# Kernel tuning notes

Hardware: AMD Instinct MI355X
Metric: run time of the kernel (lower is better)

## Reference

```python
import jax, jax.numpy as jnp
import numpy as np

NC, NP_, E = 100000, 50000, 500000
DC, DP = 256, 128
HID, OUT = 64, 64
H1, H2 = 2, 1
SLOPE = 0.2


def setup_inputs() -> dict:
    key = jax.random.key(0)
    ks = jax.random.split(key, 32)
    d = {}
    d['x_customer'] = jax.random.normal(ks[0], (NC, DC), jnp.float32)
    d['x_product'] = jax.random.normal(ks[1], (NP_, DP), jnp.float32)
    d['edge_src'] = jax.random.randint(ks[2], (E,), 0, NC, jnp.int32)
    d['edge_dst'] = jax.random.randint(ks[3], (E,), 0, NP_, jnp.int32)
    s = 0.1
    # layer1, edge type (customer, buys, product): src=customer, dst=product
    d['w1b_src'] = jax.random.normal(ks[4], (DC, H1 * HID)) * s
    d['w1b_dst'] = jax.random.normal(ks[5], (DP, H1 * HID)) * s
    d['a1b_src'] = jax.random.normal(ks[6], (H1, HID)) * s
    d['a1b_dst'] = jax.random.normal(ks[7], (H1, HID)) * s
    d['b1b'] = jnp.zeros((H1 * HID,), jnp.float32)
    # layer1, edge type (product, rev_buys, customer): src=product, dst=customer
    d['w1r_src'] = jax.random.normal(ks[8], (DP, H1 * HID)) * s
    d['w1r_dst'] = jax.random.normal(ks[9], (DC, H1 * HID)) * s
    d['a1r_src'] = jax.random.normal(ks[10], (H1, HID)) * s
    d['a1r_dst'] = jax.random.normal(ks[11], (H1, HID)) * s
    d['b1r'] = jnp.zeros((H1 * HID,), jnp.float32)
    # layer2 (input dim = H1*HID = 128 for both node types), heads=1
    d['w2b_src'] = jax.random.normal(ks[12], (H1 * HID, H2 * OUT)) * s
    d['w2b_dst'] = jax.random.normal(ks[13], (H1 * HID, H2 * OUT)) * s
    d['a2b_src'] = jax.random.normal(ks[14], (H2, OUT)) * s
    d['a2b_dst'] = jax.random.normal(ks[15], (H2, OUT)) * s
    d['b2b'] = jnp.zeros((H2 * OUT,), jnp.float32)
    d['w2r_src'] = jax.random.normal(ks[16], (H1 * HID, H2 * OUT)) * s
    d['w2r_dst'] = jax.random.normal(ks[17], (H1 * HID, H2 * OUT)) * s
    d['a2r_src'] = jax.random.normal(ks[18], (H2, OUT)) * s
    d['a2r_dst'] = jax.random.normal(ks[19], (H2, OUT)) * s
    d['b2r'] = jnp.zeros((H2 * OUT,), jnp.float32)
    return d


def _gat_conv(h_src, h_dst, e_src, e_dst, att_src, att_dst, bias, n_dst):
    # h_src: [Ns,H,C] projected source feats; h_dst: [Nd,H,C]
    a_s = (h_src * att_src).sum(-1)  # [Ns,H]
    a_d = (h_dst * att_dst).sum(-1)  # [Nd,H]
    alpha = jax.nn.leaky_relu(a_s[e_src] + a_d[e_dst], negative_slope=SLOPE)  # [E,H]
    m = jax.lax.stop_gradient(jax.ops.segment_max(alpha, e_dst, num_segments=n_dst))
    ex = jnp.exp(alpha - m[e_dst])
    den = jax.ops.segment_sum(ex, e_dst, num_segments=n_dst)
    w = ex / (den[e_dst] + 1e-16)  # segment softmax over incoming edges
    msg = h_src[e_src] * w[..., None]  # [E,H,C]
    out = jax.ops.segment_sum(msg, e_dst, num_segments=n_dst)  # [Nd,H,C]
    return out.reshape(n_dst, -1) + bias


def reference(x_customer, x_product, edge_src, edge_dst,
              w1b_src, w1b_dst, a1b_src, a1b_dst, b1b,
              w1r_src, w1r_dst, a1r_src, a1r_dst, b1r,
              w2b_src, w2b_dst, a2b_src, a2b_dst, b2b,
              w2r_src, w2r_dst, a2r_src, a2r_dst, b2r):
    # ---- layer 1 (heads=2, concat) ----
    hs = (x_customer @ w1b_src).reshape(NC, H1, HID)
    hd = (x_product @ w1b_dst).reshape(NP_, H1, HID)
    p1 = _gat_conv(hs, hd, edge_src, edge_dst, a1b_src, a1b_dst, b1b, NP_)
    hs = (x_product @ w1r_src).reshape(NP_, H1, HID)
    hd = (x_customer @ w1r_dst).reshape(NC, H1, HID)
    c1 = _gat_conv(hs, hd, edge_dst, edge_src, a1r_src, a1r_dst, b1r, NC)
    c1 = jax.nn.relu(c1)
    p1 = jax.nn.relu(p1)
    # ---- layer 2 (heads=1) ----
    hs = (c1 @ w2b_src).reshape(NC, H2, OUT)
    hd = (p1 @ w2b_dst).reshape(NP_, H2, OUT)
    p2 = _gat_conv(hs, hd, edge_src, edge_dst, a2b_src, a2b_dst, b2b, NP_)
    hs = (p1 @ w2r_src).reshape(NP_, H2, OUT)
    hd = (c1 @ w2r_dst).reshape(NC, H2, OUT)
    c2 = _gat_conv(hs, hd, edge_dst, edge_src, a2r_src, a2r_dst, b2r, NC)
    return c2, p2
```

## Files before the change

kernel.cpp:

```cpp
#include <hip/hip_runtime.h>
#include <hip/hip_bf16.h>

typedef __bf16 bf16_t;
typedef bf16_t bf16x2 __attribute__((ext_vector_type(2)));
typedef bf16_t bf16x4 __attribute__((ext_vector_type(4)));
typedef bf16_t bf16x8 __attribute__((ext_vector_type(8)));
typedef float f32x2 __attribute__((ext_vector_type(2)));
typedef float f32x4 __attribute__((ext_vector_type(4)));

static constexpr int NCn = 100000;
static constexpr int NPn = 50000;
static constexpr int NE  = 500000;

__device__ __forceinline__ float ldin(const void* p, size_t i, int fp32) {
    return fp32 ? ((const float*)p)[i] : (float)((const bf16_t*)p)[i];
}

__global__ __launch_bounds__(256) void prep_meta(const void* x, int* flag,
                                                 const void* w1bd, const void* a1bd,
                                                 const void* w1rd, const void* a1rd,
                                                 const void* w2bd, const void* a2bd,
                                                 const void* w2rd, const void* a2rd,
                                                 float* V1bd, float* V1rd,
                                                 float* V2bd, float* V2rd) {
    __shared__ int sflag;
    int t = threadIdx.x;
    if (t < 64) {
        const bf16_t* xb = (const bf16_t*)x;
        int bad = 0;
        for (int i = t; i < 512; i += 64) {
            float v = (float)xb[i];
            if (!(v > -1e4f && v < 1e4f)) bad = 1;
        }
        unsigned long long m = __ballot(bad);
        if (t == 0) { sflag = (m != 0ull) ? 1 : 0; flag[0] = sflag; }
    }
    __syncthreads();
    int fp32 = sflag;
    for (int idx = t; idx < 256; idx += 256) {
        int k = idx >> 1, h = idx & 1;
        float s = 0.f;
        for (int c = 0; c < 64; ++c)
            s += ldin(w1bd, (size_t)k * 128 + h * 64 + c, fp32) * ldin(a1bd, h * 64 + c, fp32);
        V1bd[k * 2 + h] = s;
    }
    for (int idx = t; idx < 512; idx += 256) {
        int k = idx >> 1, h = idx & 1;
        float s = 0.f;
        for (int c = 0; c < 64; ++c)
            s += ldin(w1rd, (size_t)k * 128 + h * 64 + c, fp32) * ldin(a1rd, h * 64 + c, fp32);
        V1rd[k * 2 + h] = s;
    }
    for (int k = t; k < 128; k += 256) {
        float s = 0.f;
        for (int c = 0; c < 64; ++c)
            s += ldin(w2bd, (size_t)k * 64 + c, fp32) * ldin(a2bd, c, fp32);
        V2bd[k] = s;
    }
    for (int k = t; k < 128; k += 256) {
        float s = 0.f;
        for (int c = 0; c < 64; ++c)
            s += ldin(w2rd, (size_t)k * 64 + c, fp32) * ldin(a2rd, c, fp32);
        V2rd[k] = s;
    }
}

__global__ __launch_bounds__(256) void prep_w4(const void* __restrict__ w1b, bf16_t* __restrict__ Wt1b,
                                               const void* __restrict__ w1r, bf16_t* __restrict__ Wt1r,
                                               const void* __restrict__ w2b, bf16_t* __restrict__ Wt2b,
                                               const void* __restrict__ w2r, bf16_t* __restrict__ Wt2r,
                                               const int* __restrict__ flag) {
    int fp32 = flag[0];
    int b = blockIdx.x;
    const void* W; bf16_t* Wt; int N, ks, base;
    if (b < 128)      { W = w1b; Wt = Wt1b; N = 128; ks = 8; base = 0;   }
    else if (b < 192) { W = w1r; Wt = Wt1r; N = 128; ks = 7; base = 128; }
    else if (b < 224) { W = w2b; Wt = Wt2b; N = 64;  ks = 7; base = 192; }
    else              { W = w2r; Wt = Wt2r; N = 64;  ks = 7; base = 224; }
    int idx = (b - base) * 256 + threadIdx.x;
    int K = 1 << ks;
    int n = idx >> ks, k = idx & (K - 1);
    if (n < N) Wt[idx] = (bf16_t)ldin(W, (size_t)k * N + n, fp32);
}

template<int K>
__device__ __forceinline__ void cvt_body(const void* __restrict__ X,
                                         bf16_t* __restrict__ Xb,
                                         const float* __restrict__ V,
                                         float* __restrict__ ad,
                                         int M, int fp32, int blk) {
    constexpr int EPL = K / 64;
    int wid = (blk * 256 + (int)threadIdx.x) >> 6;
    int lane = threadIdx.x & 63;
    if (wid >= M) return;
    size_t base = (size_t)wid * K + lane * EPL;
    float x[EPL];
    if constexpr (EPL == 4) {
        if (fp32) { f32x4 t = *(const f32x4*)((const float*)X + base);
#pragma unroll
            for (int j = 0; j < 4; ++j) x[j] = t[j];
        } else { bf16x4 t = *(const bf16x4*)((const bf16_t*)X + base);
#pragma unroll
            for (int j = 0; j < 4; ++j) x[j] = (float)t[j];
        }
        bf16x4 o;
#pragma unroll
        for (int j = 0; j < 4; ++j) o[j] = (bf16_t)x[j];
        *(bf16x4*)(Xb + base) = o;
    } else {
        if (fp32) { f32x2 t = *(const f32x2*)((const float*)X + base);
#pragma unroll
            for (int j = 0; j < 2; ++j) x[j] = t[j];
        } else { bf16x2 t = *(const bf16x2*)((const bf16_t*)X + base);
#pragma unroll
            for (int j = 0; j < 2; ++j) x[j] = (float)t[j];
        }
        bf16x2 o;
#pragma unroll
        for (int j = 0; j < 2; ++j) o[j] = (bf16_t)x[j];
        *(bf16x2*)(Xb + base) = o;
    }
    float a0 = 0.f, a1 = 0.f;
#pragma unroll
    for (int j = 0; j < EPL; ++j) {
        int k = lane * EPL + j;
        a0 += x[j] * V[k * 2];
        a1 += x[j] * V[k * 2 + 1];
    }
    for (int off = 32; off; off >>= 1) {
        a0 += __shfl_down(a0, off);
        a1 += __shfl_down(a1, off);
    }
    if (lane == 0) { ad[(size_t)wid * 2] = a0; ad[(size_t)wid * 2 + 1] = a1; }
}

__global__ __launch_bounds__(256) void cvt2(const void* __restrict__ Xc, bf16_t* __restrict__ Xcb,
                                            const float* __restrict__ Vc, float* __restrict__ adc,
                                            const void* __restrict__ Xp, bf16_t* __restrict__ Xpb,
                                            const float* __restrict__ Vp, float* __restrict__ adp,
                                            int gC, const int* __restrict__ flag) {
    int fp32 = flag[0];
    if ((int)blockIdx.x < gC) cvt_body<256>(Xc, Xcb, Vc, adc, NCn, fp32, blockIdx.x);
    else                      cvt_body<128>(Xp, Xpb, Vp, adp, NPn, fp32, blockIdx.x - gC);
}

__global__ __launch_bounds__(256) void zero2(int* __restrict__ a, int na,
                                             int* __restrict__ b, int nb) {
    int i = blockIdx.x * 256 + threadIdx.x;
    if (i < na) a[i] = 0;
    else if (i - na < nb) b[i - na] = 0;
}

__global__ __launch_bounds__(256) void hist2(const int* __restrict__ esrc,
                                             const int* __restrict__ edst,
                                             int* __restrict__ cntR,
                                             int* __restrict__ cntB, int E) {
    int e = blockIdx.x * 256 + threadIdx.x;
    if (e >= E) return;
    atomicAdd(&cntB[edst[e]], 1);
    atomicAdd(&cntR[esrc[e]], 1);
}

__global__ __launch_bounds__(256) void scan_blocks2(const int* __restrict__ cntB, int* __restrict__ rsB,
                                                    int* __restrict__ bsumB, int NB, int sbB,
                                                    const int* __restrict__ cntR, int* __restrict__ rsR,
                                                    int* __restrict__ bsumR, int NR) {
    const int* cnt; int* rs; int* bsum; int N; int b;
    if ((int)blockIdx.x < sbB) { cnt = cntB; rs = rsB; bsum = bsumB; N = NB; b = blockIdx.x; }
    else { cnt = cntR; rs = rsR; bsum = bsumR; N = NR; b = blockIdx.x - sbB; }
    int t = threadIdx.x;
    int base = b * 1024 + t * 4;
    int c[4];
#pragma unroll
    for (int k = 0; k < 4; ++k) { int i = base + k; c[k] = (i < N) ? cnt[i] : 0; }
    int tsum = c[0] + c[1] + c[2] + c[3];
    __shared__ int sd[256];
    sd[t] = tsum;
    __syncthreads();
    for (int off = 1; off < 256; off <<= 1) {
        int x = (t >= off) ? sd[t - off] : 0;
        __syncthreads();
        sd[t] += x;
        __syncthreads();
    }
    int run = sd[t] - tsum;
#pragma unroll
    for (int k = 0; k < 4; ++k) { int i = base + k; if (i < N) rs[i] = run; run += c[k]; }
    if (t == 255) bsum[b] = sd[255];
}

__global__ __launch_bounds__(128) void scan_bsum2(int* __restrict__ bsumB, int nbB,
                                                  int* __restrict__ bsumR, int nbR) {
    int* bsum = blockIdx.x ? bsumR : bsumB;
    int nb = blockIdx.x ? nbR : nbB;
    int t = threadIdx.x;
    __shared__ int sd[128];
    int v = (t < nb) ? bsum[t] : 0;
    sd[t] = v;
    __syncthreads();
    for (int off = 1; off < 128; off <<= 1) {
        int x = (t >= off) ? sd[t - off] : 0;
        __syncthreads();
        sd[t] += x;
        __syncthreads();
    }
    if (t < nb) bsum[t] = sd[t] - v;
}

__global__ __launch_bounds__(256) void scan_add2(int* __restrict__ rsB, const int* __restrict__ bsumB,
                                                 int NB, int* __restrict__ cntB,
                                                 int* __restrict__ rsR, const int* __restrict__ bsumR,
                                                 int NR, int* __restrict__ cntR, int E) {
    int i = blockIdx.x * 256 + threadIdx.x;
    if (i < NB) { int v = rsB[i] + bsumB[i >> 10]; rsB[i] = v; cntB[i] = v; }
    if (i < NR) { int v = rsR[i] + bsumR[i >> 10]; rsR[i] = v; cntR[i] = v; }
    if (i == 0) { rsB[NB] = E; rsR[NR] = E; }
}

__global__ __launch_bounds__(256) void scatter2(const int* __restrict__ esrc,
                                                const int* __restrict__ edst,
                                                int* __restrict__ curB, int* __restrict__ curR,
                                                int* __restrict__ srcsB, int* __restrict__ dstsB,
                                                int* __restrict__ srcsR, int* __restrict__ dstsR,
                                                int E) {
    int e = blockIdx.x * 256 + threadIdx.x;
    if (e >= E) return;
    int s = esrc[e], d = edst[e];
    int pb = atomicAdd(&curB[d], 1);
    srcsB[pb] = s; dstsB[pb] = d;
    int pr = atomicAdd(&curR[s], 1);
    srcsR[pr] = d; dstsR[pr] = s;
}

template<int K, int NT, int H>
__device__ __forceinline__ void gemm_body(const bf16_t* __restrict__ A,
                                          const bf16_t* __restrict__ Wt,
                                          bf16_t* __restrict__ C,
                                          const void* __restrict__ att,
                                          float* __restrict__ asout,
                                          int M, int fp32, int bx) {
    constexpr int N = NT * 16;
    const int w = threadIdx.x >> 6;
    const int lane = threadIdx.x & 63;
    const int lm = lane & 15;
    const int lq = lane >> 4;
    const int r0 = bx * 128 + w * 32;
    int ra0 = r0 + lm;       if (ra0 > M - 1) ra0 = M - 1;
    int ra1 = r0 + 16 + lm;  if (ra1 > M - 1) ra1 = M - 1;
    const bf16_t* A0 = A + (size_t)ra0 * K + lq * 8;
    const bf16_t* A1 = A + (size_t)ra1 * K + lq * 8;
    const bf16_t* B0 = Wt + (size_t)lm * K + lq * 8;
    f32x4 acc[2][NT] = {};
#pragma unroll
    for (int kt = 0; kt < K / 32; ++kt) {
        bf16x8 a0 = *(const bf16x8*)(A0 + kt * 32);
        bf16x8 a1 = *(const bf16x8*)(A1 + kt * 32);
#pragma unroll
        for (int nt = 0; nt < NT; ++nt) {
            bf16x8 b = *(const bf16x8*)(B0 + (size_t)nt * 16 * K + kt * 32);
            acc[0][nt] = __builtin_amdgcn_mfma_f32_16x16x32_bf16(a0, b, acc[0][nt], 0, 0, 0);
            acc[1][nt] = __builtin_amdgcn_mfma_f32_16x16x32_bf16(a1, b, acc[1][nt], 0, 0, 0);
        }
    }
#pragma unroll
    for (int rt = 0; rt < 2; ++rt) {
        const int crow0 = r0 + rt * 16 + lq * 4;
#pragma unroll
        for (int nt = 0; nt < NT; ++nt) {
            int col = nt * 16 + lm;
#pragma unroll
            for (int i = 0; i < 4; ++i) {
                int r = crow0 + i;
                if (r < M) C[(size_t)r * N + col] = (bf16_t)acc[rt][nt][i];
            }
        }
    }
    float attv[NT];
#pragma unroll
    for (int nt = 0; nt < NT; ++nt) attv[nt] = ldin(att, nt * 16 + lm, fp32);
    float p0[2][4], p1[2][4];
#pragma unroll
    for (int rt = 0; rt < 2; ++rt)
#pragma unroll
        for (int i = 0; i < 4; ++i) {
            float s0 = 0.f, s1 = 0.f;
#pragma unroll
            for (int nt = 0; nt < NT; ++nt) {
                if (H == 2 && nt >= 4) s1 += acc[rt][nt][i] * attv[nt];
                else                   s0 += acc[rt][nt][i] * attv[nt];
            }
            p0[rt][i] = s0; p1[rt][i] = s1;
        }
#pragma unroll
    for (int off = 1; off < 16; off <<= 1)
#pragma unroll
        for (int rt = 0; rt < 2; ++rt)
#pragma unroll
            for (int i = 0; i < 4; ++i) {
                p0[rt][i] += __shfl_xor(p0[rt][i], off);
                if (H == 2) p1[rt][i] += __shfl_xor(p1[rt][i], off);
            }
    if (lm == 0) {
#pragma unroll
        for (int rt = 0; rt < 2; ++rt)
#pragma unroll
            for (int i = 0; i < 4; ++i) {
                int r = r0 + rt * 16 + lq * 4 + i;
                if (r < M) {
                    asout[(size_t)r * H] = p0[rt][i];
                    if (H == 2) asout[(size_t)r * H + 1] = p1[rt][i];
                }
            }
    }
}

__global__ __launch_bounds__(256) void gemm_l1(const bf16_t* __restrict__ xcb, const bf16_t* __restrict__ Wt1b,
                                               bf16_t* __restrict__ Hc, const void* __restrict__ a1b, float* __restrict__ as_b,
                                               const bf16_t* __restrict__ xpb, const bf16_t* __restrict__ Wt1r,
                                               bf16_t* __restrict__ Hp, const void* __restrict__ a1r, float* __restrict__ as_r,
                                               int gmC, const int* __restrict__ flag) {
    int fp32 = flag[0];
    if ((int)blockIdx.x < gmC)
        gemm_body<256, 8, 2>(xcb, Wt1b, Hc, a1b, as_b, NCn, fp32, blockIdx.x);
    else
        gemm_body<128, 8, 2>(xpb, Wt1r, Hp, a1r, as_r, NPn, fp32, blockIdx.x - gmC);
}

__global__ __launch_bounds__(256) void gemm_l2(const bf16_t* __restrict__ c1, const bf16_t* __restrict__ Wt2b,
                                               bf16_t* __restrict__ Hc2, const void* __restrict__ a2b, float* __restrict__ as2c,
                                               const bf16_t* __restrict__ p1, const bf16_t* __restrict__ Wt2r,
                                               bf16_t* __restrict__ Hp2, const void* __restrict__ a2r, float* __restrict__ as2p,
                                               int gmC, const int* __restrict__ flag) {
    int fp32 = flag[0];
    if ((int)blockIdx.x < gmC)
        gemm_body<128, 4, 1>(c1, Wt2b, Hc2, a2b, as2c, NCn, fp32, blockIdx.x);
    else
        gemm_body<128, 4, 1>(p1, Wt2r, Hp2, a2r, as2p, NPn, fp32, blockIdx.x - gmC);
}

template<int H>
__global__ __launch_bounds__(256) void edge_pk2(const int* __restrict__ srcsB,
                                                const int* __restrict__ dstsB,
                                                const float* __restrict__ asB,
                                                const float* __restrict__ adB,
                                                float* __restrict__ pkB,
                                                const int* __restrict__ srcsR,
                                                const int* __restrict__ dstsR,
                                                const float* __restrict__ asR,
                                                const float* __restrict__ adR,
                                                float* __restrict__ pkR,
                                                int gE, int E) {
    const int *srcs, *dsts; const float *as_, *ad_; float* pk; int j;
    if ((int)blockIdx.x < gE) {
        j = blockIdx.x * 256 + threadIdx.x;
        srcs = srcsB; dsts = dstsB; as_ = asB; ad_ = adB; pk = pkB;
    } else {
        j = (blockIdx.x - gE) * 256 + threadIdx.x;
        srcs = srcsR; dsts = dstsR; as_ = asR; ad_ = adR; pk = pkR;
    }
    if (j >= E) return;
    int s = srcs[j], d = dsts[j];
    if constexpr (H == 2) {
        f32x2 a = *(const f32x2*)(as_ + 2 * (size_t)s);
        f32x2 b = *(const f32x2*)(ad_ + 2 * (size_t)d);
        float v0 = a[0] + b[0]; v0 = v0 > 0.f ? v0 : 0.2f * v0;
        float v1 = a[1] + b[1]; v1 = v1 > 0.f ? v1 : 0.2f * v1;
        f32x4 o;
        o[0] = __uint_as_float((unsigned)s << 8);
        o[1] = __expf(fminf(v0, 60.f));
        o[2] = __expf(fminf(v1, 60.f));
        o[3] = 0.f;
        *(f32x4*)(pk + 4 * (size_t)j) = o;
    } else {
        float v = as_[s] + ad_[d];
        v = v > 0.f ? v : 0.2f * v;
        f32x2 o;
        o[0] = __uint_as_float((unsigned)s << 7);
        o[1] = __expf(fminf(v, 60.f));
        *(f32x2*)(pk + 2 * (size_t)j) = o;
    }
}

template<int HD, int MODE>
__global__ __launch_bounds__(256) void aggregate2(
        const int* __restrict__ rsB, const float* __restrict__ pkB,
        const bf16_t* __restrict__ HmB, const void* __restrict__ biasB,
        const float* __restrict__ V2B, float* __restrict__ ad2B,
        void* __restrict__ outB, size_t obaseB, int NdB,
        const int* __restrict__ rsR, const float* __restrict__ pkR,
        const bf16_t* __restrict__ HmR, const void* __restrict__ biasR,
        const float* __restrict__ V2R, float* __restrict__ ad2R,
        void* __restrict__ outR, size_t obaseR, int NdR,
        int gB, const int* __restrict__ flag) {
    constexpr int NH = HD / 64;
    int lane = threadIdx.x & 63;
    const int* rs; const float* pk; const bf16_t* Hm;
    const void* bias; const float* V2; float* ad2; void* outb; size_t obase;
    int wid, Nd;
    if ((int)blockIdx.x < gB) {
        wid = blockIdx.x * 4 + (threadIdx.x >> 6);
        rs = rsB; pk = pkB; Hm = HmB; bias = biasB;
        V2 = V2B; ad2 = ad2B; outb = outB; obase = obaseB; Nd = NdB;
    } else {
        wid = (blockIdx.x - gB) * 4 + (threadIdx.x >> 6);
        rs = rsR; pk = pkR; Hm = HmR; bias = biasR;
        V2 = V2R; ad2 = ad2R; outb = outR; obase = obaseR; Nd = NdR;
    }
    if (wid >= Nd) return;
    int start = rs[wid], end = rs[wid + 1];
    int fp32 = flag[0];
    const int hsel = lane >> 5;

    float den = 0.f, acc0 = 0.f, acc1 = 0.f;
    if constexpr (NH == 2) {
        const unsigned loff = 4u * lane;
        const f32x4* pkv = (const f32x4*)pk;
#pragma unroll 4
        for (int j = start; j < end; ++j) {
            f32x4 e = pkv[j];
            unsigned off = __float_as_uint(e[0]) + loff;
            float eh = hsel ? e[2] : e[1];
            den += eh;
            bf16x2 hv = *(const bf16x2*)((const char*)Hm + off);
            acc0 += (float)hv[0] * eh;
            acc1 += (float)hv[1] * eh;
        }
    } else {
        const unsigned loff = 2u * lane;
        const f32x2* pkv = (const f32x2*)pk;
#pragma unroll 4
        for (int j = start; j < end; ++j) {
            f32x2 e = pkv[j];
            unsigned off = __float_as_uint(e[0]) + loff;
            float eh = e[1];
            den += eh;
            acc0 += (float)(*(const bf16_t*)((const char*)Hm + off)) * eh;
        }
    }
    float inv = 1.f / (den + 1e-16f);

    if constexpr (MODE == 0) {
        int c0 = 2 * lane;
        float o0 = fmaxf(acc0 * inv + ldin(bias, c0, fp32), 0.f);
        float o1 = fmaxf(acc1 * inv + ldin(bias, c0 + 1, fp32), 0.f);
        bf16x2 ov;
        ov[0] = (bf16_t)o0;
        ov[1] = (bf16_t)o1;
        *(bf16x2*)((bf16_t*)outb + (size_t)wid * 128 + c0) = ov;
        float pp = o0 * V2[c0] + o1 * V2[c0 + 1];
        for (int off = 32; off; off >>= 1) pp += __shfl_down(pp, off);
        if (lane == 0) ad2[wid] = pp;
    } else {
        float o = acc0 * inv + ldin(bias, lane, fp32);
        size_t oi = obase + (size_t)wid * 64 + lane;
        if (fp32) ((float*)outb)[oi] = o;
        else      ((bf16_t*)outb)[oi] = (bf16_t)o;
    }
}

extern "C" void kernel_launch(void* const* d_in, const int* in_sizes, int n_in,
                              void* d_out, int out_size, void* d_ws, size_t ws_size,
                              hipStream_t stream) {
    const void* xc = d_in[0];
    const void* xp = d_in[1];
    const int* esrc = (const int*)d_in[2];
    const int* edst = (const int*)d_in[3];
    const void* w1b_src = d_in[4];
    const void* w1b_dst = d_in[5];
    const void* a1b_src = d_in[6];
    const void* a1b_dst = d_in[7];
    const void* b1b     = d_in[8];
    const void* w1r_src = d_in[9];
    const void* w1r_dst = d_in[10];
    const void* a1r_src = d_in[11];
    const void* a1r_dst = d_in[12];
    const void* b1r     = d_in[13];
    const void* w2b_src = d_in[14];
    const void* w2b_dst = d_in[15];
    const void* a2b_src = d_in[16];
    const void* a2b_dst = d_in[17];
    const void* b2b     = d_in[18];
    const void* w2r_src = d_in[19];
    const void* w2r_dst = d_in[20];
    const void* a2r_src = d_in[21];
    const void* a2r_dst = d_in[22];
    const void* b2r     = d_in[23];

    char* p = (char*)d_ws;
    auto alloc = [&](size_t nbytes) {
        char* r = p;
        p += (nbytes + 255) & ~(size_t)255;
        return r;
    };
    int* flag   = (int*)alloc(256);
    float* V1bd = (float*)alloc(256 * 4);
    float* V1rd = (float*)alloc(512 * 4);
    float* V2bd = (float*)alloc(128 * 4);
    float* V2rd = (float*)alloc(128 * 4);
    bf16_t* Wt1b = (bf16_t*)alloc(128 * 256 * 2);
    bf16_t* Wt1r = (bf16_t*)alloc(128 * 128 * 2);
    bf16_t* Wt2b = (bf16_t*)alloc(64 * 128 * 2);
    bf16_t* Wt2r = (bf16_t*)alloc(64 * 128 * 2);
    float* as_b = (float*)alloc((size_t)NCn * 2 * 4);
    float* as_r = (float*)alloc((size_t)NPn * 2 * 4);
    float* as2_c = (float*)alloc((size_t)NCn * 4);
    float* as2_p = (float*)alloc((size_t)NPn * 4);
    float* ad_b = (float*)alloc((size_t)NPn * 2 * 4);
    float* ad_r = (float*)alloc((size_t)NCn * 2 * 4);
    float* ad2_b = (float*)alloc((size_t)NPn * 4);
    float* ad2_r = (float*)alloc((size_t)NCn * 4);
    int* rsB    = (int*)alloc((size_t)(NPn + 1) * 4);
    int* rsR    = (int*)alloc((size_t)(NCn + 1) * 4);
    int* srcsB  = (int*)alloc((size_t)NE * 4);
    int* srcsR  = (int*)alloc((size_t)NE * 4);
    int* dstsB  = (int*)alloc((size_t)NE * 4);
    int* dstsR  = (int*)alloc((size_t)NE * 4);
    float* pkB  = (float*)alloc((size_t)NE * 16);
    float* pkR  = (float*)alloc((size_t)NE * 16);
    int* cntB   = (int*)alloc((size_t)NPn * 4);
    int* cntR   = (int*)alloc((size_t)NCn * 4);
    int* bsumB  = (int*)alloc(128 * 4);
    int* bsumR  = (int*)alloc(128 * 4);
    bf16_t* xcb = (bf16_t*)alloc((size_t)NCn * 256 * 2);
    bf16_t* xpb = (bf16_t*)alloc((size_t)NPn * 128 * 2);
    bf16_t* Hc  = (bf16_t*)alloc((size_t)NCn * 128 * 2);
    bf16_t* Hp  = (bf16_t*)alloc((size_t)NPn * 128 * 2);
    bf16_t* c1  = (bf16_t*)alloc((size_t)NCn * 128 * 2);
    bf16_t* p1  = (bf16_t*)alloc((size_t)NPn * 128 * 2);
    bf16_t* Hc2 = (bf16_t*)alloc((size_t)NCn * 64 * 2);
    bf16_t* Hp2 = (bf16_t*)alloc((size_t)NPn * 64 * 2);

    const dim3 blk(256);
    const int gE = (NE + 255) / 256;
    const int sbP = (NPn + 1023) / 1024;
    const int sbR = (NCn + 1023) / 1024;
    const int gmC = (NCn + 127) / 128;
    const int gmP = (NPn + 127) / 128;
    const int gNC = (NCn + 255) / 256;
    const int gBoth = (NPn + NCn + 255) / 256;
    const int gAggB = (NPn + 3) / 4;
    const int gAggR = (NCn + 3) / 4;
    const int gCvtC = (NCn + 3) / 4;
    const int gCvtP = (NPn + 3) / 4;

    prep_meta<<<1, 256, 0, stream>>>(xc, flag, w1b_dst, a1b_dst, w1r_dst, a1r_dst,
                                     w2b_dst, a2b_dst, w2r_dst, a2r_dst,
                                     V1bd, V1rd, V2bd, V2rd);
    prep_w4<<<256, blk, 0, stream>>>(w1b_src, Wt1b, w1r_src, Wt1r,
                                     w2b_src, Wt2b, w2r_src, Wt2r, flag);

    zero2<<<gBoth, blk, 0, stream>>>(cntB, NPn, cntR, NCn);
    hist2<<<gE, blk, 0, stream>>>(esrc, edst, cntR, cntB, NE);
    scan_blocks2<<<sbP + sbR, blk, 0, stream>>>(cntB, rsB, bsumB, NPn, sbP,
                                                cntR, rsR, bsumR, NCn);
    scan_bsum2<<<2, 128, 0, stream>>>(bsumB, sbP, bsumR, sbR);
    scan_add2<<<gNC, blk, 0, stream>>>(rsB, bsumB, NPn, cntB, rsR, bsumR, NCn, cntR, NE);
    scatter2<<<gE, blk, 0, stream>>>(esrc, edst, cntB, cntR, srcsB, dstsB, srcsR, dstsR, NE);

    cvt2<<<gCvtC + gCvtP, blk, 0, stream>>>(xc, xcb, V1rd, ad_r,
                                            xp, xpb, V1bd, ad_b, gCvtC, flag);

    gemm_l1<<<gmC + gmP, blk, 0, stream>>>(xcb, Wt1b, Hc, a1b_src, as_b,
                                           xpb, Wt1r, Hp, a1r_src, as_r,
                                           gmC, flag);

    edge_pk2<2><<<2 * gE, blk, 0, stream>>>(srcsB, dstsB, as_b, ad_b, pkB,
                                            srcsR, dstsR, as_r, ad_r, pkR, gE, NE);
    aggregate2<128, 0><<<gAggB + gAggR, blk, 0, stream>>>(
        rsB, pkB, Hc, b1b, V2bd, ad2_b, p1, 0, NPn,
        rsR, pkR, Hp, b1r, V2rd, ad2_r, c1, 0, NCn, gAggB, flag);

    gemm_l2<<<gmC + gmP, blk, 0, stream>>>(c1, Wt2b, Hc2, a2b_src, as2_c,
                                           p1, Wt2r, Hp2, a2r_src, as2_p,
                                           gmC, flag);

    edge_pk2<1><<<2 * gE, blk, 0, stream>>>(srcsB, dstsB, as2_c, ad2_b, pkB,
                                            srcsR, dstsR, as2_p, ad2_r, pkR, gE, NE);
    aggregate2<64, 1><<<gAggB + gAggR, blk, 0, stream>>>(
        rsB, pkB, Hc2, b2b, nullptr, nullptr, d_out, (size_t)NCn * 64, NPn,
        rsR, pkR, Hp2, b2r, nullptr, nullptr, d_out, 0, NCn, gAggB, flag);
}
```

Baseline: 602.1 us.

## Process two destination nodes per wavefront in aggregation, split edges across half-waves

```diff
diff --git a/kernel.cpp b/kernel.cpp
--- a/kernel.cpp
+++ b/kernel.cpp
@@ -392,69 +392,140 @@
         const float* __restrict__ V2R, float* __restrict__ ad2R,
         void* __restrict__ outR, size_t obaseR, int NdR,
         int gB, const int* __restrict__ flag) {
-    constexpr int NH = HD / 64;
     int lane = threadIdx.x & 63;
     const int* rs; const float* pk; const bf16_t* Hm;
     const void* bias; const float* V2; float* ad2; void* outb; size_t obase;
-    int wid, Nd;
+    int wpair, Nd;
     if ((int)blockIdx.x < gB) {
-        wid = blockIdx.x * 4 + (threadIdx.x >> 6);
+        wpair = (blockIdx.x * 4 + (threadIdx.x >> 6)) * 2;
         rs = rsB; pk = pkB; Hm = HmB; bias = biasB;
         V2 = V2B; ad2 = ad2B; outb = outB; obase = obaseB; Nd = NdB;
     } else {
-        wid = (blockIdx.x - gB) * 4 + (threadIdx.x >> 6);
+        wpair = ((blockIdx.x - gB) * 4 + (threadIdx.x >> 6)) * 2;
         rs = rsR; pk = pkR; Hm = HmR; bias = biasR;
         V2 = V2R; ad2 = ad2R; outb = outR; obase = obaseR; Nd = NdR;
     }
-    if (wid >= Nd) return;
-    int start = rs[wid], end = rs[wid + 1];
+    int widA = wpair, widB = wpair + 1;
+    if (widA >= Nd) return;
+    int startA = rs[widA], endA = rs[widA + 1];
+    int startB = endA;
+    int endB = (widB < Nd) ? rs[widB + 1] : endA;
     int fp32 = flag[0];
-    const int hsel = lane >> 5;
-
-    float den = 0.f, acc0 = 0.f, acc1 = 0.f;
-    if constexpr (NH == 2) {
+
+    if constexpr (MODE == 0) {
+        const int hsel = lane >> 5;
         const unsigned loff = 4u * lane;
         const f32x4* pkv = (const f32x4*)pk;
-#pragma unroll 4
-        for (int j = start; j < end; ++j) {
-            f32x4 e = pkv[j];
-            unsigned off = __float_as_uint(e[0]) + loff;
-            float eh = hsel ? e[2] : e[1];
-            den += eh;
-            bf16x2 hv = *(const bf16x2*)((const char*)Hm + off);
-            acc0 += (float)hv[0] * eh;
-            acc1 += (float)hv[1] * eh;
+        float denA = 0.f, aA0 = 0.f, aA1 = 0.f;
+        float denB = 0.f, aB0 = 0.f, aB1 = 0.f;
+        int nA = endA - startA, nB = endB - startB;
+        int n = nA > nB ? nA : nB;
+#pragma unroll 2
+        for (int it = 0; it < n; ++it) {
+            if (it < nA) {
+                f32x4 e = pkv[startA + it];
+                unsigned off = __float_as_uint(e[0]) + loff;
+                float eh = hsel ? e[2] : e[1];
+                denA += eh;
+                bf16x2 hv = *(const bf16x2*)((const char*)Hm + off);
+                aA0 += (float)hv[0] * eh;
+                aA1 += (float)hv[1] * eh;
+            }
+            if (it < nB) {
+                f32x4 e = pkv[startB + it];
+                unsigned off = __float_as_uint(e[0]) + loff;
+                float eh = hsel ? e[2] : e[1];
+                denB += eh;
+                bf16x2 hv = *(const bf16x2*)((const char*)Hm + off);
+                aB0 += (float)hv[0] * eh;
+                aB1 += (float)hv[1] * eh;
+            }
+        }
+        float invA = 1.f / (denA + 1e-16f);
+        float invB = 1.f / (denB + 1e-16f);
+        int c0 = 2 * lane;
+        float b0 = ldin(bias, c0, fp32), b1 = ldin(bias, c0 + 1, fp32);
+        float v20 = V2[c0], v21 = V2[c0 + 1];
+        float oA0 = fmaxf(aA0 * invA + b0, 0.f);
+        float oA1 = fmaxf(aA1 * invA + b1, 0.f);
+        float oB0 = fmaxf(aB0 * invB + b0, 0.f);
+        float oB1 = fmaxf(aB1 * invB + b1, 0.f);
+        bf16x2 ovA; ovA[0] = (bf16_t)oA0; ovA[1] = (bf16_t)oA1;
+        *(bf16x2*)((bf16_t*)outb + (size_t)widA * 128 + c0) = ovA;
+        if (widB < Nd) {
+            bf16x2 ovB; ovB[0] = (bf16_t)oB0; ovB[1] = (bf16_t)oB1;
+            *(bf16x2*)((bf16_t*)outb + (size_t)widB * 128 + c0) = ovB;
+        }
+        float ppA = oA0 * v20 + oA1 * v21;
+        float ppB = oB0 * v20 + oB1 * v21;
+        for (int off = 32; off; off >>= 1) {
+            ppA += __shfl_down(ppA, off);
+            ppB += __shfl_down(ppB, off);
+        }
+        if (lane == 0) {
+            ad2[widA] = ppA;
+            if (widB < Nd) ad2[widB] = ppB;
         }
     } else {
-        const unsigned loff = 2u * lane;
+        const int half = lane >> 5;
+        const int l31 = lane & 31;
+        const unsigned loff = 4u * l31;
         const f32x2* pkv = (const f32x2*)pk;
-#pragma unroll 4
-        for (int j = start; j < end; ++j) {
-            f32x2 e = pkv[j];
-            unsigned off = __float_as_uint(e[0]) + loff;
-            float eh = e[1];
-            den += eh;
-            acc0 += (float)(*(const bf16_t*)((const char*)Hm + off)) * eh;
-        }
-    }
-    float inv = 1.f / (den + 1e-16f);
-
-    if constexpr (MODE == 0) {
-        int c0 = 2 * lane;
-        float o0 = fmaxf(acc0 * inv + ldin(bias, c0, fp32), 0.f);
-        float o1 = fmaxf(acc1 * inv + ldin(bias, c0 + 1, fp32), 0.f);
-        bf16x2 ov;
-        ov[0] = (bf16_t)o0;
-        ov[1] = (bf16_t)o1;
-        *(bf16x2*)((bf16_t*)outb + (size_t)wid * 128 + c0) = ov;
-        float pp = o0 * V2[c0] + o1 * V2[c0 + 1];
-        for (int off = 32; off; off >>= 1) pp += __shfl_down(pp, off);
-        if (lane == 0) ad2[wid] = pp;
-    } else {
-        float o = acc0 * inv + ldin(bias, lane, fp32);
-        size_t oi = obase + (size_t)wid * 64 + lane;
-        if (fp32) ((float*)outb)[oi] = o;
-        else      ((bf16_t*)outb)[oi] = (bf16_t)o;
+        float denA = 0.f, aA0 = 0.f, aA1 = 0.f;
+        float denB = 0.f, aB0 = 0.f, aB1 = 0.f;
+        int nA = endA - startA, nB = endB - startB;
+        int nmax = nA > nB ? nA : nB;
+        int n = (nmax + 1) >> 1;
+#pragma unroll 2
+        for (int it = 0; it < n; ++it) {
+            int jA = startA + 2 * it + half;
+            if (jA < endA) {
+                f32x2 e = pkv[jA];
+                unsigned off = __float_as_uint(e[0]) + loff;
+                float eh = e[1];
+                denA += eh;
+                bf16x2 hv = *(const bf16x2*)((const char*)Hm + off);
+                aA0 += (float)hv[0] * eh;
+                aA1 += (float)hv[1] * eh;
+            }
+            int jB = startB + 2 * it + half;
+            if (jB < endB) {
+                f32x2 e = pkv[jB];
+                unsigned off = __float_as_uint(e[0]) + loff;
+                float eh = e[1];
+                denB += eh;
+                bf16x2 hv = *(const bf16x2*)((const char*)Hm + off);
+                aB0 += (float)hv[0] * eh;
+                aB1 += (float)hv[1] * eh;
+            }
+        }
+        aA0 += __shfl_xor(aA0, 32); aA1 += __shfl_xor(aA1, 32);
+        denA += __shfl_xor(denA, 32);
+        aB0 += __shfl_xor(aB0, 32); aB1 += __shfl_xor(aB1, 32);
+        denB += __shfl_xor(denB, 32);
+        float invA = 1.f / (denA + 1e-16f);
+        float invB = 1.f / (denB + 1e-16f);
+        int c0 = 2 * l31;
+        float b0 = ldin(bias, c0, fp32), b1 = ldin(bias, c0 + 1, fp32);
+        float oA0 = aA0 * invA + b0, oA1 = aA1 * invA + b1;
+        float oB0 = aB0 * invB + b0, oB1 = aB1 * invB + b1;
+        if (lane < 32) {
+            if (fp32) {
+                f32x2 ov; ov[0] = oA0; ov[1] = oA1;
+                *(f32x2*)((float*)outb + obase + (size_t)widA * 64 + c0) = ov;
+                if (widB < Nd) {
+                    f32x2 ow; ow[0] = oB0; ow[1] = oB1;
+                    *(f32x2*)((float*)outb + obase + (size_t)widB * 64 + c0) = ow;
+                }
+            } else {
+                bf16x2 ov; ov[0] = (bf16_t)oA0; ov[1] = (bf16_t)oA1;
+                *(bf16x2*)((bf16_t*)outb + obase + (size_t)widA * 64 + c0) = ov;
+                if (widB < Nd) {
+                    bf16x2 ow; ow[0] = (bf16_t)oB0; ow[1] = (bf16_t)oB1;
+                    *(bf16x2*)((bf16_t*)outb + obase + (size_t)widB * 64 + c0) = ow;
+                }
+            }
+        }
     }
 }
 
@@ -538,8 +609,8 @@
     const int gmP = (NPn + 127) / 128;
     const int gNC = (NCn + 255) / 256;
     const int gBoth = (NPn + NCn + 255) / 256;
-    const int gAggB = (NPn + 3) / 4;
-    const int gAggR = (NCn + 3) / 4;
+    const int gAggB = (NPn + 7) / 8;
+    const int gAggR = (NCn + 7) / 8;
     const int gCvtC = (NCn + 3) / 4;
     const int gCvtP = (NPn + 3) / 4;
 
```

New measurement: 637.9 us. 5.9% more time.
